# Performance work log

Measured on AMD Instinct MI355X. Metric: run time of the kernel, lower is better.

## Reference

```python
import jax, jax.numpy as jnp
import numpy as np
import math

EPS_LN = 1e-5
SCALE = 16.0  # cosine_sim_scale


def layer_norm(x, g):
    mean = jnp.mean(x, axis=-1, keepdims=True)
    var = jnp.var(x, axis=-1, keepdims=True)  # biased, matches unbiased=False
    return (x - mean) * jax.lax.rsqrt(var + EPS_LN) * g


def l2norm(t):
    n = jnp.linalg.norm(t, axis=-1, keepdims=True)
    return t / jnp.maximum(n, 1e-12)


def setup_inputs() -> dict:
    key = jax.random.key(0)
    ks = jax.random.split(key, 4)
    b, n, dim, h, dh = 4, 2048, 1024, 8, 64
    inner = h * dh
    x = jax.random.normal(ks[0], (b, n, dim), dtype=jnp.float32)
    Wq = jax.random.normal(ks[1], (dim, inner), dtype=jnp.float32) * (dim ** -0.5)
    Wkv = jax.random.normal(ks[2], (dim, 2 * dh), dtype=jnp.float32) * (dim ** -0.5)
    Wout = jax.random.normal(ks[3], (inner, dim), dtype=jnp.float32) * (inner ** -0.5)
    norm_g = jnp.ones((dim,), dtype=jnp.float32)
    out_norm_g = jnp.ones((dim,), dtype=jnp.float32)
    return {"x": x, "norm_g": norm_g, "Wq": Wq, "Wkv": Wkv, "Wout": Wout,
            "out_norm_g": out_norm_g}


def reference(x, norm_g, Wq, Wkv, Wout, out_norm_g):
    b, n, dim = x.shape
    h = 8
    dh = Wkv.shape[-1] // 2
    xn = layer_norm(x, norm_g)
    q = xn @ Wq                      # [b, n, h*dh]
    kv = xn @ Wkv                    # [b, n, 2*dh]
    k, v = kv[..., :dh], kv[..., dh:]
    q = q.reshape(b, n, h, dh).transpose(0, 2, 1, 3)  # [b, h, n, dh]
    q = q * SCALE                    # cancelled by l2norm, kept for fidelity
    q = l2norm(q)
    k = l2norm(k)
    rs = math.sqrt(SCALE)
    q = q * rs
    k = k * rs
    sim = jnp.einsum('bhid,bjd->bhij', q, k)          # [b, h, n, n]
    attn = jax.nn.softmax(sim.astype(jnp.float32), axis=-1).astype(sim.dtype)
    out = jnp.einsum('bhij,bjd->bhid', attn, v)       # [b, h, n, dh]
    out = out.transpose(0, 2, 1, 3).reshape(b, n, h * dh)
    out = out @ Wout
    return layer_norm(out, out_norm_g)
```

## Files before the change

### kernel.cpp

```cpp
#include <hip/hip_runtime.h>
#include <hip/hip_bf16.h>

typedef __attribute__((ext_vector_type(8))) short short8;
typedef __attribute__((ext_vector_type(4))) float floatx4;

__device__ __forceinline__ float bf2f(ushort u) {
    return __uint_as_float(((unsigned int)u) << 16);
}
__device__ __forceinline__ ushort f2bf(float f) {
    unsigned int u = __float_as_uint(f);
    unsigned int r = (u + 0x7FFFu + ((u >> 16) & 1u)) >> 16;
    return (ushort)r;
}
__device__ __forceinline__ unsigned int pk2(float a, float b) {
    union { __hip_bfloat162 h; unsigned int u; } cv;
    cv.h = __float22bfloat162_rn(make_float2(a, b));
    return cv.u;
}
__device__ __forceinline__ float scrub(float v, float lim) {
    return fminf(fmaxf(v, -lim), lim);
}
__device__ __forceinline__ void glds16(const ushort* g, ushort* l) {
    __builtin_amdgcn_global_load_lds((const __attribute__((address_space(1))) void*)g,
                                     (__attribute__((address_space(3))) void*)l, 16, 0, 0);
}

__device__ __forceinline__ bool detect_bf16(const ushort* __restrict__ probe) {
    const int lane = threadIdx.x & 63;
    ushort u = probe[(lane & 31) * 2];
    int e = (u >> 7) & 0xFF;
    bool pl = (e >= 117) && (e <= 131) && (lane < 32);
    return __popcll(__ballot(pl)) >= 16;
}

__device__ __forceinline__ void do_transpose(const void* __restrict__ in,
                                             ushort* __restrict__ out,
                                             int bx, int by, int in_rs, int out_rs,
                                             bool ib, ushort* tile ) {
    const int tx = threadIdx.x & 31, ty = threadIdx.x >> 5;
    #pragma unroll
    for (int rr = 0; rr < 32; rr += 8) {
        size_t idx = (size_t)(by * 32 + ty + rr) * in_rs + bx * 32 + tx;
        float v = ib ? bf2f(((const ushort*)in)[idx]) : ((const float*)in)[idx];
        tile[(ty + rr) * 33 + tx] = f2bf(scrub(v, 1e8f));
    }
    __syncthreads();
    #pragma unroll
    for (int rr = 0; rr < 32; rr += 8) {
        int r = bx * 32 + ty + rr;
        int c = by * 32 + tx;
        out[(size_t)r * out_rs + c] = tile[tx * 33 + (ty + rr)];
    }
}

__global__ __launch_bounds__(256) void prep_kernel(const void* __restrict__ xin,
                                                   const void* __restrict__ gin,
                                                   const void* __restrict__ Wq,
                                                   const void* __restrict__ Wkv,
                                                   ushort* __restrict__ xn,
                                                   ushort* __restrict__ wcatT,
                                                   const ushort* __restrict__ probe) {
    const bool ib = detect_bf16(probe);
    const int id = blockIdx.x;
    __shared__ ushort tile[32 * 33];
    __shared__ float red[8];

    if (id >= 8192) {
        if (id < 8704) {
            int t = id - 8192;
            do_transpose(Wq, wcatT, t & 15, t >> 4, 512, 1024, ib, tile);
        } else {
            int t = id - 8704;
            do_transpose(Wkv, wcatT + (size_t)512 * 1024, t & 3, t >> 2, 128, 1024, ib, tile);
        }
        return;
    }

    const int row = id;
    const int tid = threadIdx.x;
    float v0, v1, v2, v3, g0, g1, g2, g3;
    if (ib) {
        uint2 u = *(const uint2*)((const ushort*)xin + (size_t)row * 1024 + tid * 4);
        v0 = bf2f((ushort)(u.x & 0xFFFF)); v1 = bf2f((ushort)(u.x >> 16));
        v2 = bf2f((ushort)(u.y & 0xFFFF)); v3 = bf2f((ushort)(u.y >> 16));
        uint2 gu = *(const uint2*)((const ushort*)gin + tid * 4);
        g0 = bf2f((ushort)(gu.x & 0xFFFF)); g1 = bf2f((ushort)(gu.x >> 16));
        g2 = bf2f((ushort)(gu.y & 0xFFFF)); g3 = bf2f((ushort)(gu.y >> 16));
    } else {
        float4 xv = *(const float4*)((const float*)xin + (size_t)row * 1024 + tid * 4);
        v0 = xv.x; v1 = xv.y; v2 = xv.z; v3 = xv.w;
        float4 gv = *(const float4*)((const float*)gin + tid * 4);
        g0 = gv.x; g1 = gv.y; g2 = gv.z; g3 = gv.w;
    }
    v0 = scrub(v0, 1e8f); v1 = scrub(v1, 1e8f); v2 = scrub(v2, 1e8f); v3 = scrub(v3, 1e8f);
    g0 = scrub(g0, 1e8f); g1 = scrub(g1, 1e8f); g2 = scrub(g2, 1e8f); g3 = scrub(g3, 1e8f);

    float s  = v0 + v1 + v2 + v3;
    float sq = v0 * v0 + v1 * v1 + v2 * v2 + v3 * v3;
    #pragma unroll
    for (int off = 1; off < 64; off <<= 1) {
        s  += __shfl_xor(s, off);
        sq += __shfl_xor(sq, off);
    }
    const int w = tid >> 6, lane = tid & 63;
    if (lane == 0) { red[w] = s; red[w + 4] = sq; }
    __syncthreads();
    float S  = red[0] + red[1] + red[2] + red[3];
    float SQ = red[4] + red[5] + red[6] + red[7];

    float mean = S * (1.0f / 1024.0f);
    float var  = SQ * (1.0f / 1024.0f) - mean * mean;
    float rstd = rsqrtf(fmaxf(var, 0.0f) + 1e-5f);

    uint2 ov;
    ov.x = pk2((v0 - mean) * rstd * g0, (v1 - mean) * rstd * g1);
    ov.y = pk2((v2 - mean) * rstd * g2, (v3 - mean) * rstd * g3);
    *(uint2*)(xn + (size_t)row * 1024 + tid * 4) = ov;
}

__global__ __launch_bounds__(256) void wout_tr_kernel(const void* __restrict__ Wout,
                                                      ushort* __restrict__ woT,
                                                      const ushort* __restrict__ probe) {
    const bool ib = detect_bf16(probe);
    __shared__ ushort tile[32 * 33];
    do_transpose(Wout, woT, blockIdx.x, blockIdx.y, 1024, 512, ib, tile);
}

__global__ __launch_bounds__(256) void ln2_kernel(const ushort* __restrict__ y,
                                                  const void* __restrict__ gin,
                                                  void* __restrict__ out,
                                                  const ushort* __restrict__ probe) {
    const bool ob = detect_bf16(probe);
    const int row = blockIdx.x;
    const int tid = threadIdx.x;

    uint2 u = *(const uint2*)(y + (size_t)row * 1024 + tid * 4);
    float v0 = scrub(bf2f((ushort)(u.x & 0xFFFF)), 1e8f);
    float v1 = scrub(bf2f((ushort)(u.x >> 16)),    1e8f);
    float v2 = scrub(bf2f((ushort)(u.y & 0xFFFF)), 1e8f);
    float v3 = scrub(bf2f((ushort)(u.y >> 16)),    1e8f);

    float g0, g1, g2, g3;
    if (ob) {
        uint2 gu = *(const uint2*)((const ushort*)gin + tid * 4);
        g0 = bf2f((ushort)(gu.x & 0xFFFF)); g1 = bf2f((ushort)(gu.x >> 16));
        g2 = bf2f((ushort)(gu.y & 0xFFFF)); g3 = bf2f((ushort)(gu.y >> 16));
    } else {
        float4 gv = *(const float4*)((const float*)gin + tid * 4);
        g0 = gv.x; g1 = gv.y; g2 = gv.z; g3 = gv.w;
    }
    g0 = scrub(g0, 1e8f); g1 = scrub(g1, 1e8f); g2 = scrub(g2, 1e8f); g3 = scrub(g3, 1e8f);

    float s  = v0 + v1 + v2 + v3;
    float sq = v0 * v0 + v1 * v1 + v2 * v2 + v3 * v3;
    #pragma unroll
    for (int off = 1; off < 64; off <<= 1) {
        s  += __shfl_xor(s, off);
        sq += __shfl_xor(sq, off);
    }
    __shared__ float red[8];
    const int w = tid >> 6, lane = tid & 63;
    if (lane == 0) { red[w] = s; red[w + 4] = sq; }
    __syncthreads();
    float S  = red[0] + red[1] + red[2] + red[3];
    float SQ = red[4] + red[5] + red[6] + red[7];

    float mean = S * (1.0f / 1024.0f);
    float var  = SQ * (1.0f / 1024.0f) - mean * mean;
    float rstd = rsqrtf(fmaxf(var, 0.0f) + 1e-5f);

    float o0 = (v0 - mean) * rstd * g0;
    float o1 = (v1 - mean) * rstd * g1;
    float o2 = (v2 - mean) * rstd * g2;
    float o3 = (v3 - mean) * rstd * g3;
    if (ob) {
        uint2 ov;
        ov.x = pk2(o0, o1);
        ov.y = pk2(o2, o3);
        *(uint2*)((ushort*)out + (size_t)row * 1024 + tid * 4) = ov;
    } else {
        *(float4*)((float*)out + (size_t)row * 1024 + tid * 4) = make_float4(o0, o1, o2, o3);
    }
}

__global__ __launch_bounds__(256) void gemm_qkv(const ushort* __restrict__ A,
                                                const ushort* __restrict__ Bt,
                                                ushort* __restrict__ qb,
                                                ushort* __restrict__ kb,
                                                ushort* __restrict__ vt) {
    __shared__ ushort a_t[64 * 32];
    __shared__ ushort b_t[64 * 32];

    const int bx = blockIdx.x;
    const int n0 = bx * 64, m0 = blockIdx.y * 64;
    const int tid = threadIdx.x;
    const int w = tid >> 6, lane = tid & 63;
    const int fm = lane & 15, quad = lane >> 4;
    const int K = 1024;

    const ushort* ag = A + (size_t)(m0 + (tid >> 2)) * K + (tid & 3) * 8;
    const ushort* bg = Bt + (size_t)(n0 + (tid >> 2)) * K + (tid & 3) * 8;
    ushort* la = a_t + w * 512;
    ushort* lb = b_t + w * 512;

    floatx4 acc[4];
    floatx4 zero4 = {0.0f, 0.0f, 0.0f, 0.0f};
    #pragma unroll
    for (int nt = 0; nt < 4; nt++) acc[nt] = zero4;

    union U8 { uint4 u4; short8 s8; };

    for (int k0 = 0; k0 < K; k0 += 32) {
        __syncthreads();
        glds16(ag + k0, la);
        glds16(bg + k0, lb);
        __syncthreads();

        U8 af;
        af.u4 = *(const uint4*)&a_t[(w * 16 + fm) * 32 + quad * 8];
        #pragma unroll
        for (int nt = 0; nt < 4; nt++) {
            U8 bf;
            bf.u4 = *(const uint4*)&b_t[(nt * 16 + fm) * 32 + quad * 8];
            acc[nt] = __builtin_amdgcn_mfma_f32_16x16x32_bf16(af.s8, bf.s8, acc[nt], 0, 0, 0);
        }
    }

    if (bx < 9) {
        float sc[4];
        #pragma unroll
        for (int r = 0; r < 4; r++) {
            float ss = acc[0][r] * acc[0][r] + acc[1][r] * acc[1][r]
                     + acc[2][r] * acc[2][r] + acc[3][r] * acc[3][r];
            ss += __shfl_xor(ss, 1);
            ss += __shfl_xor(ss, 2);
            ss += __shfl_xor(ss, 4);
            ss += __shfl_xor(ss, 8);
            sc[r] = 4.0f / fmaxf(sqrtf(ss), 1e-12f);
        }
        ushort* op;
        int rs;
        if (bx < 8) { op = qb + n0; rs = 512; }
        else        { op = kb;      rs = 64;  }
        #pragma unroll
        for (int nt = 0; nt < 4; nt++)
            #pragma unroll
            for (int r = 0; r < 4; r++)
                op[(size_t)(m0 + w * 16 + quad * 4 + r) * rs + nt * 16 + fm] =
                    f2bf(acc[nt][r] * sc[r]);
    } else {
        const int b = m0 >> 11;
        const int jb = (m0 & 2047) + w * 16 + quad * 4;
        ushort* vb = vt + (size_t)b * 64 * 2048 + jb;
        #pragma unroll
        for (int nt = 0; nt < 4; nt++) {
            uint2 pv;
            pv.x = pk2(acc[nt][0], acc[nt][1]);
            pv.y = pk2(acc[nt][2], acc[nt][3]);
            *(uint2*)(vb + (size_t)(nt * 16 + fm) * 2048) = pv;
        }
    }
}

__global__ __launch_bounds__(256) void gemm_bt128(const ushort* __restrict__ A,
                                                  const ushort* __restrict__ Bt,
                                                  ushort* __restrict__ C,
                                                  int M, int N, int K) {
    __shared__ ushort a_t[128][32];
    __shared__ ushort b_t[128][32];

    const int n0 = blockIdx.x * 128, m0 = blockIdx.y * 128;
    const int tid = threadIdx.x;
    const int w = tid >> 6, lane = tid & 63;
    const int fm = lane & 15, quad = lane >> 4;

    const int c0 = tid, c1 = tid + 256;
    const ushort* ag0 = A + (size_t)(m0 + (c0 >> 2)) * K + (c0 & 3) * 8;
    const ushort* ag1 = A + (size_t)(m0 + (c1 >> 2)) * K + (c1 & 3) * 8;
    const ushort* bg0 = Bt + (size_t)(n0 + (c0 >> 2)) * K + (c0 & 3) * 8;
    const ushort* bg1 = Bt + (size_t)(n0 + (c1 >> 2)) * K + (c1 & 3) * 8;
    ushort* la0 = &a_t[0][0] + w * 512;
    ushort* la1 = &a_t[0][0] + 2048 + w * 512;
    ushort* lb0 = &b_t[0][0] + w * 512;
    ushort* lb1 = &b_t[0][0] + 2048 + w * 512;

    floatx4 acc[2][8];
    floatx4 zero4 = {0.0f, 0.0f, 0.0f, 0.0f};
    #pragma unroll
    for (int mt = 0; mt < 2; mt++)
        #pragma unroll
        for (int nt = 0; nt < 8; nt++) acc[mt][nt] = zero4;

    union U8 { uint4 u4; short8 s8; };

    for (int k0 = 0; k0 < K; k0 += 32) {
        __syncthreads();
        glds16(ag0 + k0, la0);
        glds16(ag1 + k0, la1);
        glds16(bg0 + k0, lb0);
        glds16(bg1 + k0, lb1);
        __syncthreads();

        U8 af[2];
        #pragma unroll
        for (int mt = 0; mt < 2; mt++)
            af[mt].u4 = *(const uint4*)&a_t[w * 32 + mt * 16 + fm][quad * 8];
        #pragma unroll
        for (int nt = 0; nt < 8; nt++) {
            U8 bf;
            bf.u4 = *(const uint4*)&b_t[nt * 16 + fm][quad * 8];
            acc[0][nt] = __builtin_amdgcn_mfma_f32_16x16x32_bf16(af[0].s8, bf.s8, acc[0][nt], 0, 0, 0);
            acc[1][nt] = __builtin_amdgcn_mfma_f32_16x16x32_bf16(af[1].s8, bf.s8, acc[1][nt], 0, 0, 0);
        }
    }

    #pragma unroll
    for (int mt = 0; mt < 2; mt++)
        #pragma unroll
        for (int nt = 0; nt < 8; nt++)
            #pragma unroll
            for (int r = 0; r < 4; r++)
                C[(size_t)(m0 + w * 32 + mt * 16 + quad * 4 + r) * N + n0 + nt * 16 + fm] =
                    f2bf(acc[mt][nt][r]);
}

__global__ __launch_bounds__(512, 4) void attn_kernel(const ushort* __restrict__ q,
                                                      const ushort* __restrict__ kb,
                                                      const ushort* __restrict__ vt,
                                                      ushort* __restrict__ out) {
    __shared__ ushort k_t[64 * 64];
    __shared__ ushort v_t[64 * 64];
    __shared__ ushort p_tile[8][16][72];

    const int i0 = blockIdx.x * 128;
    const int h = blockIdx.y, b = blockIdx.z;
    const int tid = threadIdx.x, w = tid >> 6, lane = tid & 63;
    const int fm = lane & 15, quad = lane >> 4;
    const int fx = fm & 7;

    union U8 { uint4 u4; short8 s8; };

    const ushort* qbase = q + ((size_t)(b * 2048 + i0 + w * 16 + fm) * 512) + h * 64 + quad * 8;
    U8 qf0, qf1;
    qf0.u4 = *(const uint4*)qbase;
    qf1.u4 = *(const uint4*)(qbase + 32);

    floatx4 zero4 = {0.0f, 0.0f, 0.0f, 0.0f};
    floatx4 acc_o[4];
    #pragma unroll
    for (int od = 0; od < 4; od++) acc_o[od] = zero4;
    float lsum = 0.0f;

    const ushort* kbb = kb + (size_t)b * 2048 * 64;
    const ushort* vtb = vt + (size_t)b * 64 * 2048;

    const int srow = w * 8 + (lane >> 3);
    const int soct = (lane & 7) ^ ((lane >> 3) & 7);
    const ushort* kgl = kbb + (size_t)srow * 64 + soct * 8;
    const ushort* vgl = vtb + (size_t)srow * 2048 + soct * 8;
    ushort* kld = k_t + w * 512;
    ushort* vld = v_t + w * 512;

    const int o0 = (quad ^ fx) * 8;
    const int o1 = ((quad + 4) ^ fx) * 8;

    for (int j0 = 0; j0 < 2048; j0 += 64) {
        __syncthreads();
        glds16(kgl + (size_t)j0 * 64, kld);
        glds16(vgl + j0, vld);
        __syncthreads();

        #pragma unroll
        for (int nt = 0; nt < 4; nt++) {
            const int kr = (nt * 16 + fm) * 64;
            U8 kf0, kf1;
            kf0.u4 = *(const uint4*)&k_t[kr + o0];
            kf1.u4 = *(const uint4*)&k_t[kr + o1];
            floatx4 st = zero4;
            st = __builtin_amdgcn_mfma_f32_16x16x32_bf16(kf0.s8, qf0.s8, st, 0, 0, 0);
            st = __builtin_amdgcn_mfma_f32_16x16x32_bf16(kf1.s8, qf1.s8, st, 0, 0, 0);
            float p0 = __expf(st[0] - 16.0f);
            float p1 = __expf(st[1] - 16.0f);
            float p2 = __expf(st[2] - 16.0f);
            float p3 = __expf(st[3] - 16.0f);
            lsum += (p0 + p1) + (p2 + p3);
            uint2 pkv;
            pkv.x = pk2(p0, p1);
            pkv.y = pk2(p2, p3);
            *(uint2*)&p_tile[w][fm][nt * 16 + quad * 4] = pkv;
        }

        U8 pb0, pb1;
        pb0.u4 = *(const uint4*)&p_tile[w][fm][quad * 8];
        pb1.u4 = *(const uint4*)&p_tile[w][fm][32 + quad * 8];

        #pragma unroll
        for (int od = 0; od < 4; od++) {
            const int vr = (od * 16 + fm) * 64;
            U8 vf0, vf1;
            vf0.u4 = *(const uint4*)&v_t[vr + o0];
            vf1.u4 = *(const uint4*)&v_t[vr + o1];
            acc_o[od] = __builtin_amdgcn_mfma_f32_16x16x32_bf16(vf0.s8, pb0.s8, acc_o[od], 0, 0, 0);
            acc_o[od] = __builtin_amdgcn_mfma_f32_16x16x32_bf16(vf1.s8, pb1.s8, acc_o[od], 0, 0, 0);
        }
    }

    lsum += __shfl_xor(lsum, 16);
    lsum += __shfl_xor(lsum, 32);
    float li = 1.0f / fmaxf(lsum, 1e-30f);

    ushort* ob = out + (size_t)(b * 2048 + i0 + w * 16 + fm) * 512 + h * 64;
    #pragma unroll
    for (int od = 0; od < 4; od++) {
        uint2 ov;
        ov.x = pk2(acc_o[od][0] * li, acc_o[od][1] * li);
        ov.y = pk2(acc_o[od][2] * li, acc_o[od][3] * li);
        *(uint2*)(ob + od * 16 + quad * 4) = ov;
    }
}

extern "C" void kernel_launch(void* const* d_in, const int* in_sizes, int n_in,
                              void* d_out, int out_size, void* d_ws, size_t ws_size,
                              hipStream_t stream) {
    const void* x          = d_in[0];
    const void* norm_g     = d_in[1];
    const void* Wq         = d_in[2];
    const void* Wkv        = d_in[3];
    const void* Wout       = d_in[4];
    const void* out_norm_g = d_in[5];
    const ushort* probe = (const ushort*)d_in[0];
    ushort* ws = (ushort*)d_ws;

    const size_t M1 = 1024 * 1024 / 2;
    ushort* xn    = (ushort*)d_out;
    ushort* ao    = (ushort*)d_out;
    ushort* woT   = (ushort*)((char*)d_out + (8u << 20));
    ushort* qb    = ws;
    ushort* kb    = ws + 8 * M1;
    ushort* vt    = ws + 9 * M1;
    ushort* wcatT = ws + 11 * M1;
    ushort* y     = ws;

    prep_kernel<<<8832, 256, 0, stream>>>(x, norm_g, Wq, Wkv, xn, wcatT, probe);

    gemm_qkv<<<dim3(10, 128), 256, 0, stream>>>(xn, wcatT, qb, kb, vt);

    wout_tr_kernel<<<dim3(32, 16), 256, 0, stream>>>(Wout, woT, probe);

    attn_kernel<<<dim3(16, 8, 4), 512, 0, stream>>>(qb, kb, vt, ao);

    gemm_bt128<<<dim3(8, 64), 256, 0, stream>>>(ao, woT, y, 8192, 1024, 512);

    ln2_kernel<<<8192, 256, 0, stream>>>(y, out_norm_g, d_out, probe);
}
```

Before: 212.2 us.

## Double-buffer K/V tiles and keep softmax probabilities in registers

The attention kernel now uses two LDS buffers for K and V, issuing the next tile's async global-to-LDS load before computing on the current one. This halves the barriers per tile and overlaps memory with MFMA work. It also drops the per-wave P staging tile: K rows are permuted at load time so each lane's S accumulators line up with the B-operand layout the PV MFMA needs, and P is packed to bf16 in registers. This removes LDS round trips but adds LDS footprint and depends on the permutation being correct.

```diff
diff --git a/kernel.cpp b/kernel.cpp
--- a/kernel.cpp
+++ b/kernel.cpp
@@ -328,9 +328,8 @@
                                                       const ushort* __restrict__ kb,
                                                       const ushort* __restrict__ vt,
                                                       ushort* __restrict__ out) {
-    __shared__ ushort k_t[64 * 64];
-    __shared__ ushort v_t[64 * 64];
-    __shared__ ushort p_tile[8][16][72];
+    __shared__ ushort k_t[2][64 * 64];
+    __shared__ ushort v_t[2][64 * 64];
 
     const int i0 = blockIdx.x * 128;
     const int h = blockIdx.y, b = blockIdx.z;
@@ -355,54 +354,72 @@
     const ushort* vtb = vt + (size_t)b * 64 * 2048;
 
     const int srow = w * 8 + (lane >> 3);
-    const int soct = (lane & 7) ^ ((lane >> 3) & 7);
-    const ushort* kgl = kbb + (size_t)srow * 64 + soct * 8;
+    const int soct = (lane & 7) ^ (srow & 7);
+    const int pm = ((srow >> 4) & 1) * 32 + ((srow >> 2) & 3) * 8
+                 + (srow >> 5) * 4 + (srow & 3);
+    const ushort* kgl = kbb + (size_t)pm * 64 + soct * 8;
     const ushort* vgl = vtb + (size_t)srow * 2048 + soct * 8;
-    ushort* kld = k_t + w * 512;
-    ushort* vld = v_t + w * 512;
+    ushort* kld0 = k_t[0] + w * 512;
+    ushort* vld0 = v_t[0] + w * 512;
+    ushort* kld1 = k_t[1] + w * 512;
+    ushort* vld1 = v_t[1] + w * 512;
 
     const int o0 = (quad ^ fx) * 8;
     const int o1 = ((quad + 4) ^ fx) * 8;
 
-    for (int j0 = 0; j0 < 2048; j0 += 64) {
-        __syncthreads();
-        glds16(kgl + (size_t)j0 * 64, kld);
-        glds16(vgl + j0, vld);
-        __syncthreads();
-
+    auto compute = [&](const ushort* kt, const ushort* vtl) {
+        float p[4][4];
         #pragma unroll
         for (int nt = 0; nt < 4; nt++) {
             const int kr = (nt * 16 + fm) * 64;
             U8 kf0, kf1;
-            kf0.u4 = *(const uint4*)&k_t[kr + o0];
-            kf1.u4 = *(const uint4*)&k_t[kr + o1];
+            kf0.u4 = *(const uint4*)&kt[kr + o0];
+            kf1.u4 = *(const uint4*)&kt[kr + o1];
             floatx4 st = zero4;
             st = __builtin_amdgcn_mfma_f32_16x16x32_bf16(kf0.s8, qf0.s8, st, 0, 0, 0);
             st = __builtin_amdgcn_mfma_f32_16x16x32_bf16(kf1.s8, qf1.s8, st, 0, 0, 0);
-            float p0 = __expf(st[0] - 16.0f);
-            float p1 = __expf(st[1] - 16.0f);
-            float p2 = __expf(st[2] - 16.0f);
-            float p3 = __expf(st[3] - 16.0f);
-            lsum += (p0 + p1) + (p2 + p3);
-            uint2 pkv;
-            pkv.x = pk2(p0, p1);
-            pkv.y = pk2(p2, p3);
-            *(uint2*)&p_tile[w][fm][nt * 16 + quad * 4] = pkv;
-        }
-
+            #pragma unroll
+            for (int r = 0; r < 4; r++) {
+                p[nt][r] = __expf(st[r] - 16.0f);
+                lsum += p[nt][r];
+            }
+        }
         U8 pb0, pb1;
-        pb0.u4 = *(const uint4*)&p_tile[w][fm][quad * 8];
-        pb1.u4 = *(const uint4*)&p_tile[w][fm][32 + quad * 8];
-
+        pb0.u4.x = pk2(p[0][0], p[0][1]);
+        pb0.u4.y = pk2(p[0][2], p[0][3]);
+        pb0.u4.z = pk2(p[2][0], p[2][1]);
+        pb0.u4.w = pk2(p[2][2], p[2][3]);
+        pb1.u4.x = pk2(p[1][0], p[1][1]);
+        pb1.u4.y = pk2(p[1][2], p[1][3]);
+        pb1.u4.z = pk2(p[3][0], p[3][1]);
+        pb1.u4.w = pk2(p[3][2], p[3][3]);
         #pragma unroll
         for (int od = 0; od < 4; od++) {
             const int vr = (od * 16 + fm) * 64;
             U8 vf0, vf1;
-            vf0.u4 = *(const uint4*)&v_t[vr + o0];
-            vf1.u4 = *(const uint4*)&v_t[vr + o1];
+            vf0.u4 = *(const uint4*)&vtl[vr + o0];
+            vf1.u4 = *(const uint4*)&vtl[vr + o1];
             acc_o[od] = __builtin_amdgcn_mfma_f32_16x16x32_bf16(vf0.s8, pb0.s8, acc_o[od], 0, 0, 0);
             acc_o[od] = __builtin_amdgcn_mfma_f32_16x16x32_bf16(vf1.s8, pb1.s8, acc_o[od], 0, 0, 0);
         }
+    };
+
+    glds16(kgl, kld0);
+    glds16(vgl, vld0);
+    __syncthreads();
+
+    for (int j0 = 0; j0 < 2048; j0 += 128) {
+        glds16(kgl + (size_t)(j0 + 64) * 64, kld1);
+        glds16(vgl + (j0 + 64), vld1);
+        compute(k_t[0], v_t[0]);
+        __syncthreads();
+
+        if (j0 + 128 < 2048) {
+            glds16(kgl + (size_t)(j0 + 128) * 64, kld0);
+            glds16(vgl + (j0 + 128), vld0);
+        }
+        compute(k_t[1], v_t[1]);
+        __syncthreads();
     }
 
     lsum += __shfl_xor(lsum, 16);
```

After: 210.2 us. About the same (-1.0%).

## Restructure attention with 32x32 MFMA, double-buffered KV, split-K waves, exp2 softmax

Applied to the files above, without the earlier changes.

Rewrites the attention kernel around 32x32x16 MFMAs. P stays in registers as the B operand of the PV product, so the LDS round trip for the probability tile goes away. The K/V tiles are double-buffered so global-to-LDS loads overlap compute, and the two halves of the key sequence are split across wave groups and reduced through LDS at the end. The q scale is folded into log2e in the projection epilogue so the kernel can use exp2f with a constant bias. The cost is higher register and LDS use and an extra cross-wave reduction.

```diff
diff --git a/kernel.cpp b/kernel.cpp
--- a/kernel.cpp
+++ b/kernel.cpp
@@ -3,6 +3,7 @@
 
 typedef __attribute__((ext_vector_type(8))) short short8;
 typedef __attribute__((ext_vector_type(4))) float floatx4;
+typedef __attribute__((ext_vector_type(16))) float floatx16;
 
 __device__ __forceinline__ float bf2f(ushort u) {
     return __uint_as_float(((unsigned int)u) << 16);
@@ -227,6 +228,7 @@
     }
 
     if (bx < 9) {
+        const float qsc = (bx < 8) ? 5.7707801636f : 4.0f;
         float sc[4];
         #pragma unroll
         for (int r = 0; r < 4; r++) {
@@ -236,7 +238,7 @@
             ss += __shfl_xor(ss, 2);
             ss += __shfl_xor(ss, 4);
             ss += __shfl_xor(ss, 8);
-            sc[r] = 4.0f / fmaxf(sqrtf(ss), 1e-12f);
+            sc[r] = qsc / fmaxf(sqrtf(ss), 1e-12f);
         }
         ushort* op;
         int rs;
@@ -328,94 +330,161 @@
                                                       const ushort* __restrict__ kb,
                                                       const ushort* __restrict__ vt,
                                                       ushort* __restrict__ out) {
-    __shared__ ushort k_t[64 * 64];
-    __shared__ ushort v_t[64 * 64];
-    __shared__ ushort p_tile[8][16][72];
+    __shared__ ushort k_t[2][2][64 * 64];
+    __shared__ ushort v_t[2][2][64 * 64];
 
     const int i0 = blockIdx.x * 128;
-    const int h = blockIdx.y, b = blockIdx.z;
+    const int h0 = blockIdx.y, b = blockIdx.z;
     const int tid = threadIdx.x, w = tid >> 6, lane = tid & 63;
-    const int fm = lane & 15, quad = lane >> 4;
-    const int fx = fm & 7;
+    const int qg = w & 3;
+    const int kh = w >> 2;
+    const int cq = lane & 31;
+    const int hi = lane >> 5;
+    const int sw = cq & 7;
 
     union U8 { uint4 u4; short8 s8; };
 
-    const ushort* qbase = q + ((size_t)(b * 2048 + i0 + w * 16 + fm) * 512) + h * 64 + quad * 8;
-    U8 qf0, qf1;
-    qf0.u4 = *(const uint4*)qbase;
-    qf1.u4 = *(const uint4*)(qbase + 32);
-
-    floatx4 zero4 = {0.0f, 0.0f, 0.0f, 0.0f};
-    floatx4 acc_o[4];
-    #pragma unroll
-    for (int od = 0; od < 4; od++) acc_o[od] = zero4;
+    const ushort* qbase = q + (size_t)(b * 2048 + i0 + qg * 32 + cq) * 512 + h0 * 64 + hi * 8;
+    U8 qf[4];
+    #pragma unroll
+    for (int dm = 0; dm < 4; dm++) qf[dm].u4 = *(const uint4*)(qbase + dm * 16);
+
+    floatx16 acc0, acc1;
+    #pragma unroll
+    for (int i = 0; i < 16; i++) { acc0[i] = 0.0f; acc1[i] = 0.0f; }
     float lsum = 0.0f;
 
     const ushort* kbb = kb + (size_t)b * 2048 * 64;
     const ushort* vtb = vt + (size_t)b * 64 * 2048;
 
     const int srow = w * 8 + (lane >> 3);
-    const int soct = (lane & 7) ^ ((lane >> 3) & 7);
-    const ushort* kgl = kbb + (size_t)srow * 64 + soct * 8;
+    const int soct = (lane & 7) ^ (srow & 7);
+    const int prow = (srow & ~12) | ((srow & 4) << 1) | ((srow & 8) >> 1);
+    const ushort* kgl = kbb + (size_t)prow * 64 + soct * 8;
     const ushort* vgl = vtb + (size_t)srow * 2048 + soct * 8;
-    ushort* kld = k_t + w * 512;
-    ushort* vld = v_t + w * 512;
-
-    const int o0 = (quad ^ fx) * 8;
-    const int o1 = ((quad + 4) ^ fx) * 8;
-
-    for (int j0 = 0; j0 < 2048; j0 += 64) {
+    ushort* kldb = &k_t[0][0][0] + w * 512;
+    ushort* vldb = &v_t[0][0][0] + w * 512;
+
+    int koff[4];
+    #pragma unroll
+    for (int i = 0; i < 4; i++) koff[i] = ((2 * i + hi) ^ sw) * 8;
+    const int rb0 = cq * 64, rb1 = rb0 + 2048;
+
+    auto compute = [&](const ushort* ktile, const ushort* vtile) {
+        U8 pb0, pb1, pb2, pb3;
+        {
+            floatx16 st;
+            #pragma unroll
+            for (int i = 0; i < 16; i++) st[i] = -23.0831206f;
+            #pragma unroll
+            for (int dm = 0; dm < 4; dm++) {
+                U8 kf;
+                kf.u4 = *(const uint4*)&ktile[rb0 + koff[dm]];
+                st = __builtin_amdgcn_mfma_f32_32x32x16_bf16(kf.s8, qf[dm].s8, st, 0, 0, 0);
+            }
+            float p_[16];
+            #pragma unroll
+            for (int r = 0; r < 16; r++) p_[r] = exp2f(st[r]);
+            lsum += (((p_[0] + p_[1]) + (p_[2] + p_[3])) + ((p_[4] + p_[5]) + (p_[6] + p_[7])))
+                  + (((p_[8] + p_[9]) + (p_[10] + p_[11])) + ((p_[12] + p_[13]) + (p_[14] + p_[15])));
+            pb0.u4.x = pk2(p_[0], p_[1]);   pb0.u4.y = pk2(p_[2], p_[3]);
+            pb0.u4.z = pk2(p_[4], p_[5]);   pb0.u4.w = pk2(p_[6], p_[7]);
+            pb1.u4.x = pk2(p_[8], p_[9]);   pb1.u4.y = pk2(p_[10], p_[11]);
+            pb1.u4.z = pk2(p_[12], p_[13]); pb1.u4.w = pk2(p_[14], p_[15]);
+        }
+        {
+            floatx16 st;
+            #pragma unroll
+            for (int i = 0; i < 16; i++) st[i] = -23.0831206f;
+            #pragma unroll
+            for (int dm = 0; dm < 4; dm++) {
+                U8 kf;
+                kf.u4 = *(const uint4*)&ktile[rb1 + koff[dm]];
+                st = __builtin_amdgcn_mfma_f32_32x32x16_bf16(kf.s8, qf[dm].s8, st, 0, 0, 0);
+            }
+            float p_[16];
+            #pragma unroll
+            for (int r = 0; r < 16; r++) p_[r] = exp2f(st[r]);
+            lsum += (((p_[0] + p_[1]) + (p_[2] + p_[3])) + ((p_[4] + p_[5]) + (p_[6] + p_[7])))
+                  + (((p_[8] + p_[9]) + (p_[10] + p_[11])) + ((p_[12] + p_[13]) + (p_[14] + p_[15])));
+            pb2.u4.x = pk2(p_[0], p_[1]);   pb2.u4.y = pk2(p_[2], p_[3]);
+            pb2.u4.z = pk2(p_[4], p_[5]);   pb2.u4.w = pk2(p_[6], p_[7]);
+            pb3.u4.x = pk2(p_[8], p_[9]);   pb3.u4.y = pk2(p_[10], p_[11]);
+            pb3.u4.z = pk2(p_[12], p_[13]); pb3.u4.w = pk2(p_[14], p_[15]);
+        }
+        U8 vf;
+        vf.u4 = *(const uint4*)&vtile[rb0 + koff[0]];
+        acc0 = __builtin_amdgcn_mfma_f32_32x32x16_bf16(vf.s8, pb0.s8, acc0, 0, 0, 0);
+        vf.u4 = *(const uint4*)&vtile[rb0 + koff[1]];
+        acc0 = __builtin_amdgcn_mfma_f32_32x32x16_bf16(vf.s8, pb1.s8, acc0, 0, 0, 0);
+        vf.u4 = *(const uint4*)&vtile[rb0 + koff[2]];
+        acc0 = __builtin_amdgcn_mfma_f32_32x32x16_bf16(vf.s8, pb2.s8, acc0, 0, 0, 0);
+        vf.u4 = *(const uint4*)&vtile[rb0 + koff[3]];
+        acc0 = __builtin_amdgcn_mfma_f32_32x32x16_bf16(vf.s8, pb3.s8, acc0, 0, 0, 0);
+        vf.u4 = *(const uint4*)&vtile[rb1 + koff[0]];
+        acc1 = __builtin_amdgcn_mfma_f32_32x32x16_bf16(vf.s8, pb0.s8, acc1, 0, 0, 0);
+        vf.u4 = *(const uint4*)&vtile[rb1 + koff[1]];
+        acc1 = __builtin_amdgcn_mfma_f32_32x32x16_bf16(vf.s8, pb1.s8, acc1, 0, 0, 0);
+        vf.u4 = *(const uint4*)&vtile[rb1 + koff[2]];
+        acc1 = __builtin_amdgcn_mfma_f32_32x32x16_bf16(vf.s8, pb2.s8, acc1, 0, 0, 0);
+        vf.u4 = *(const uint4*)&vtile[rb1 + koff[3]];
+        acc1 = __builtin_amdgcn_mfma_f32_32x32x16_bf16(vf.s8, pb3.s8, acc1, 0, 0, 0);
+    };
+
+    glds16(kgl, kldb);
+    glds16(kgl + (size_t)1024 * 64, kldb + 4096);
+    glds16(vgl, vldb);
+    glds16(vgl + 1024, vldb + 4096);
+    __syncthreads();
+
+    const ushort* mk = &k_t[0][0][0] + kh * 4096;
+    const ushort* mv = &v_t[0][0][0] + kh * 4096;
+
+    for (int s = 0; s < 16; s++) {
+        const int cur = (s & 1) << 13;
+        const int nxt = cur ^ 8192;
+        if (s < 15) {
+            const int j = (s + 1) * 64;
+            glds16(kgl + (size_t)j * 64, kldb + nxt);
+            glds16(kgl + (size_t)(1024 + j) * 64, kldb + nxt + 4096);
+            glds16(vgl + j, vldb + nxt);
+            glds16(vgl + 1024 + j, vldb + nxt + 4096);
+        }
+        compute(mk + cur, mv + cur);
         __syncthreads();
-        glds16(kgl + (size_t)j0 * 64, kld);
-        glds16(vgl + j0, vld);
-        __syncthreads();
-
-        #pragma unroll
-        for (int nt = 0; nt < 4; nt++) {
-            const int kr = (nt * 16 + fm) * 64;
-            U8 kf0, kf1;
-            kf0.u4 = *(const uint4*)&k_t[kr + o0];
-            kf1.u4 = *(const uint4*)&k_t[kr + o1];
-            floatx4 st = zero4;
-            st = __builtin_amdgcn_mfma_f32_16x16x32_bf16(kf0.s8, qf0.s8, st, 0, 0, 0);
-            st = __builtin_amdgcn_mfma_f32_16x16x32_bf16(kf1.s8, qf1.s8, st, 0, 0, 0);
-            float p0 = __expf(st[0] - 16.0f);
-            float p1 = __expf(st[1] - 16.0f);
-            float p2 = __expf(st[2] - 16.0f);
-            float p3 = __expf(st[3] - 16.0f);
-            lsum += (p0 + p1) + (p2 + p3);
-            uint2 pkv;
-            pkv.x = pk2(p0, p1);
-            pkv.y = pk2(p2, p3);
-            *(uint2*)&p_tile[w][fm][nt * 16 + quad * 4] = pkv;
-        }
-
-        U8 pb0, pb1;
-        pb0.u4 = *(const uint4*)&p_tile[w][fm][quad * 8];
-        pb1.u4 = *(const uint4*)&p_tile[w][fm][32 + quad * 8];
-
-        #pragma unroll
-        for (int od = 0; od < 4; od++) {
-            const int vr = (od * 16 + fm) * 64;
-            U8 vf0, vf1;
-            vf0.u4 = *(const uint4*)&v_t[vr + o0];
-            vf1.u4 = *(const uint4*)&v_t[vr + o1];
-            acc_o[od] = __builtin_amdgcn_mfma_f32_16x16x32_bf16(vf0.s8, pb0.s8, acc_o[od], 0, 0, 0);
-            acc_o[od] = __builtin_amdgcn_mfma_f32_16x16x32_bf16(vf1.s8, pb1.s8, acc_o[od], 0, 0, 0);
-        }
-    }
-
-    lsum += __shfl_xor(lsum, 16);
+    }
+
+    float* xa = (float*)&k_t[0][0][0];
+    float* xb = (float*)&v_t[0][0][0];
+    if (kh == 1) {
+        float* da = xa + (qg * 64 + lane) * 18;
+        float* db = xb + (qg * 64 + lane) * 18;
+        #pragma unroll
+        for (int i = 0; i < 16; i++) { da[i] = acc0[i]; db[i] = acc1[i]; }
+        da[16] = lsum;
+    }
+    __syncthreads();
+    if (kh == 1) return;
+    {
+        const float* sa = xa + (qg * 64 + lane) * 18;
+        const float* sb = xb + (qg * 64 + lane) * 18;
+        #pragma unroll
+        for (int i = 0; i < 16; i++) { acc0[i] += sa[i]; acc1[i] += sb[i]; }
+        lsum += sa[16];
+    }
     lsum += __shfl_xor(lsum, 32);
     float li = 1.0f / fmaxf(lsum, 1e-30f);
 
-    ushort* ob = out + (size_t)(b * 2048 + i0 + w * 16 + fm) * 512 + h * 64;
-    #pragma unroll
-    for (int od = 0; od < 4; od++) {
+    ushort* ob = out + (size_t)(b * 2048 + i0 + qg * 32 + cq) * 512 + h0 * 64 + hi * 4;
+    #pragma unroll
+    for (int t = 0; t < 4; t++) {
         uint2 ov;
-        ov.x = pk2(acc_o[od][0] * li, acc_o[od][1] * li);
-        ov.y = pk2(acc_o[od][2] * li, acc_o[od][3] * li);
-        *(uint2*)(ob + od * 16 + quad * 4) = ov;
+        ov.x = pk2(acc0[4 * t] * li, acc0[4 * t + 1] * li);
+        ov.y = pk2(acc0[4 * t + 2] * li, acc0[4 * t + 3] * li);
+        *(uint2*)(ob + t * 8) = ov;
+        ov.x = pk2(acc1[4 * t] * li, acc1[4 * t + 1] * li);
+        ov.y = pk2(acc1[4 * t + 2] * li, acc1[4 * t + 3] * li);
+        *(uint2*)(ob + 32 + t * 8) = ov;
     }
 }
 
```

After: 248.2 us. 16.9% more time.
